# Kernel tuning notes

Measured on AMD Instinct MI355X. Metric: run time of the kernel, lower is better.

## Reference

```python
import jax, jax.numpy as jnp
import numpy as np

N = 50000      # nodes
E = 800000     # edges (avg degree 16)
F_IN = 64      # node_feature_dim
D = 128        # hidden_dim == output_dim
L = 3          # num_gnn_layers
B = 8          # number of graphs in the batch
GATE_H = 128   # GraphAttentionPool hidden_dim default


def _ln(x, g, b, eps=1e-5):
    m = x.mean(-1, keepdims=True)
    v = ((x - m) ** 2).mean(-1, keepdims=True)
    return (x - m) * jax.lax.rsqrt(v + eps) * g + b


def _gelu(x):
    return jax.nn.gelu(x, approximate=False)  # torch F.gelu default = exact erf


def setup_inputs() -> dict:
    key = jax.random.key(0)
    ks = jax.random.split(key, 12)
    p = lambda k, shape: (jax.random.normal(k, shape, jnp.float32) * 0.02)
    return {
        "x": jax.random.normal(ks[0], (N, F_IN), jnp.float32),
        "edge_index": jax.random.randint(ks[1], (2, E), 0, N, dtype=jnp.int32),
        "batch": jnp.sort(jax.random.randint(ks[2], (N,), 0, B, dtype=jnp.int32)),
        # input_proj: Linear + LayerNorm
        "w_in": p(ks[3], (F_IN, D)), "b_in": jnp.zeros((D,), jnp.float32),
        "ln_in_g": jnp.ones((D,), jnp.float32), "ln_in_b": jnp.zeros((D,), jnp.float32),
        # fallback GNN layers (stacked: all layers are 2D -> D)
        "gnn_w": p(ks[4], (L, 2 * D, D)), "gnn_b": jnp.zeros((L, D), jnp.float32),
        "gnn_ln_g": jnp.ones((L, D), jnp.float32), "gnn_ln_b": jnp.zeros((L, D), jnp.float32),
        # outer per-layer norms
        "norm_g": jnp.ones((L, D), jnp.float32), "norm_b": jnp.zeros((L, D), jnp.float32),
        # attention pool gate: Linear(D,128) -> tanh -> Linear(128,1)
        "gate_w1": p(ks[5], (D, GATE_H)), "gate_b1": jnp.zeros((GATE_H,), jnp.float32),
        "gate_w2": p(ks[6], (GATE_H,)), "gate_b2": jnp.zeros((), jnp.float32),
        # out_proj: Linear + LayerNorm + GELU
        "out_w": p(ks[7], (D, D)), "out_b": jnp.zeros((D,), jnp.float32),
        "out_ln_g": jnp.ones((D,), jnp.float32), "out_ln_b": jnp.zeros((D,), jnp.float32),
    }


def reference(x, edge_index, batch, w_in, b_in, ln_in_g, ln_in_b,
              gnn_w, gnn_b, gnn_ln_g, gnn_ln_b, norm_g, norm_b,
              gate_w1, gate_b1, gate_w2, gate_b2,
              out_w, out_b, out_ln_g, out_ln_b):
    src, dst = edge_index[0], edge_index[1]
    n = x.shape[0]

    # input_proj: Linear -> LayerNorm -> GELU
    h = _gelu(_ln(x @ w_in + b_in, ln_in_g, ln_in_b))

    # in-degree count (same every layer), clamped to >= 1
    deg = jax.ops.segment_sum(jnp.ones((src.shape[0],), h.dtype), dst, num_segments=n)
    deg = jnp.maximum(deg, 1.0)[:, None]  # (N, 1)

    for i in range(L):
        # mean-neighbor aggregation: gather x[src], scatter-add to dst
        agg = jax.ops.segment_sum(h[src], dst, num_segments=n) / deg  # (N, D)
        out = jnp.concatenate([h, agg], axis=-1) @ gnn_w[i] + gnn_b[i]
        h_new = _ln(_gelu(out), gnn_ln_g[i], gnn_ln_b[i])   # layer-internal norm
        h_new = _ln(h_new, norm_g[i], norm_b[i])             # outer norm
        if i < L - 1:
            h_new = _gelu(h_new) + h                         # residual (shapes match)
        h = h_new

    # attention pool (fallback path: global softmax over all nodes)
    gate_logits = jnp.tanh(h @ gate_w1 + gate_b1) @ gate_w2 + gate_b2  # (N,)
    gate = jax.nn.softmax(gate_logits, axis=0)
    pooled = jax.ops.segment_sum(h * gate[:, None], batch, num_segments=B)  # (B, D)

    spatial_embedding = _gelu(_ln(pooled @ out_w + out_b, out_ln_g, out_ln_b))
    return spatial_embedding, h, gate
```

## Files before the change

### kernel.cpp

```cpp
#include <hip/hip_runtime.h>
#include <math.h>

#define N_NODES 50000
#define N_EDGES 800000
#define F_IN 64
#define D 128
#define NLAYER 3
#define B_GRAPHS 8
#define GB 32
#define NPW 8
#define NBLK ((N_NODES + GB - 1) / GB)
#define SCAN_B 512
#define NPART ((N_NODES + SCAN_B - 1) / SCAN_B)
#define AGP 136

typedef float f32x4 __attribute__((ext_vector_type(4)));
typedef short bf16x8 __attribute__((ext_vector_type(8)));

__device__ __forceinline__ float gelu_exact(float x) {
    return 0.5f * x * (1.0f + erff(x * 0.7071067811865476f));
}

__device__ __forceinline__ unsigned short f2bf(float f) {
    unsigned int u = __float_as_uint(f);
    u = (u + 0x7fffu + ((u >> 16) & 1u)) >> 16;
    return (unsigned short)u;
}
__device__ __forceinline__ float bf2f(unsigned short u) {
    return __uint_as_float((unsigned int)u << 16);
}


__global__ void zero_int_kernel(int* __restrict__ p, int n) {
    int i = blockIdx.x * blockDim.x + threadIdx.x;
    int stride = gridDim.x * blockDim.x;
    for (; i < n; i += stride) p[i] = 0;
}

__global__ void degree_kernel(const int* __restrict__ dst, int* __restrict__ deg) {
    int e = blockIdx.x * blockDim.x + threadIdx.x;
    if (e < N_EDGES) atomicAdd(&deg[dst[e]], 1);
}

__global__ __launch_bounds__(SCAN_B) void scan_partials_kernel(const int* __restrict__ deg,
                                                               int* __restrict__ partials) {
    __shared__ int wsum[8];
    int tid = threadIdx.x;
    int lane = tid & 63, wave = tid >> 6;
    int i = blockIdx.x * SCAN_B + tid;
    int v = (i < N_NODES) ? deg[i] : 0;
    #pragma unroll
    for (int o = 32; o >= 1; o >>= 1) v += __shfl_xor(v, o);
    if (lane == 0) wsum[wave] = v;
    __syncthreads();
    if (tid == 0) {
        int t = 0;
        #pragma unroll
        for (int w = 0; w < 8; ++w) t += wsum[w];
        partials[blockIdx.x] = t;
    }
}

__global__ void scan_offsets_kernel(int* __restrict__ partials, int* __restrict__ row_ptr) {
    __shared__ int wtot[2];
    int tid = threadIdx.x;
    int lane = tid & 63, wave = tid >> 6;
    int v = (tid < NPART) ? partials[tid] : 0;
    int x = v;
    #pragma unroll
    for (int o = 1; o < 64; o <<= 1) { int nb = __shfl_up(x, o); if (lane >= o) x += nb; }
    if (lane == 63) wtot[wave] = x;
    __syncthreads();
    if (wave == 1) x += wtot[0];
    if (tid < NPART) partials[tid] = x - v;
    if (tid == 127) row_ptr[N_NODES] = x;
}

__global__ __launch_bounds__(SCAN_B) void scan_apply_kernel(const int* __restrict__ deg,
        const int* __restrict__ partials, int* __restrict__ row_ptr, int* __restrict__ cursor) {
    __shared__ int wsum[8];
    int tid = threadIdx.x;
    int lane = tid & 63, wave = tid >> 6;
    int i = blockIdx.x * SCAN_B + tid;
    int v = (i < N_NODES) ? deg[i] : 0;
    int x = v;
    #pragma unroll
    for (int o = 1; o < 64; o <<= 1) { int nb = __shfl_up(x, o); if (lane >= o) x += nb; }
    if (lane == 63) wsum[wave] = x;
    __syncthreads();
    int waveoff = 0;
    #pragma unroll
    for (int w = 0; w < 8; ++w) waveoff += (w < wave) ? wsum[w] : 0;
    int excl = partials[blockIdx.x] + waveoff + x - v;
    if (i < N_NODES) { row_ptr[i] = excl; cursor[i] = excl; }
}

__global__ void fill_kernel(const int* __restrict__ src, const int* __restrict__ dst,
                            int* __restrict__ cursor, int* __restrict__ csr) {
    int e = blockIdx.x * blockDim.x + threadIdx.x;
    if (e < N_EDGES) {
        int t = dst[e];
        int pos = atomicAdd(&cursor[t], 1);
        csr[pos] = src[e];
    }
}

#define WT_GNN (NLAYER * D * 2 * D)
#define WT_G1  (WT_GNN + D * D)
#define WT_ALL (WT_G1 + D * F_IN)
__global__ void wprep_kernel(const float* __restrict__ gnn_w, const float* __restrict__ gate_w1,
                             const float* __restrict__ w_in, unsigned short* __restrict__ wt,
                             float* __restrict__ pooled) {
    int idx = blockIdx.x * 256 + threadIdx.x;
    if (blockIdx.x == 0) {
        #pragma unroll
        for (int i = 0; i < 4; ++i) pooled[threadIdx.x + i * 256] = 0.f;
    }
    if (idx >= WT_ALL) return;
    if (idx < WT_GNN) {
        int l = idx / (D * 2 * D);
        int rem = idx - l * (D * 2 * D);
        int n = rem / (2 * D);
        int k = rem - n * (2 * D);
        wt[idx] = f2bf(gnn_w[(size_t)l * 2 * D * D + (size_t)k * D + n]);
    } else if (idx < WT_G1) {
        int rem = idx - WT_GNN;
        int n = rem / D;
        int k = rem - n * D;
        wt[idx] = f2bf(gate_w1[(size_t)k * D + n]);
    } else {
        int rem = idx - WT_G1;
        int n = rem / F_IN;
        int k = rem - n * F_IN;
        wt[idx] = f2bf(w_in[(size_t)k * D + n]);
    }
}


__global__ __launch_bounds__(256) void input_proj_v5(
        const float* __restrict__ x, const unsigned short* __restrict__ wti,
        const float* __restrict__ b, const float* __restrict__ gam,
        const float* __restrict__ bet, unsigned short* __restrict__ h16) {
    __shared__ float2 red[2][GB];
    int tid = threadIdx.x;
    int wave = tid >> 6, lane = tid & 63;
    int nblk0 = blockIdx.x * GB;
    int q = lane >> 4, c = lane & 15;
    int m0 = (wave >> 1) * 16;
    int n0 = (wave & 1) * 64;
    int mrow = nblk0 + m0 + c;
    int mclamp = (mrow < N_NODES) ? mrow : (N_NODES - 1);
    const float* xr = x + (size_t)mclamp * F_IN;

    f32x4 acc[4];
    #pragma unroll
    for (int t = 0; t < 4; ++t) {
        float bn = b[n0 + t * 16 + c];
        acc[t] = (f32x4){bn, bn, bn, bn};
    }
    #pragma unroll
    for (int kk = 0; kk < 2; ++kk) {
        float4 a0 = *(const float4*)&xr[kk * 32 + q * 8];
        float4 a1 = *(const float4*)&xr[kk * 32 + q * 8 + 4];
        bf16x8 av;
        av[0] = (short)f2bf(a0.x); av[1] = (short)f2bf(a0.y);
        av[2] = (short)f2bf(a0.z); av[3] = (short)f2bf(a0.w);
        av[4] = (short)f2bf(a1.x); av[5] = (short)f2bf(a1.y);
        av[6] = (short)f2bf(a1.z); av[7] = (short)f2bf(a1.w);
        #pragma unroll
        for (int t = 0; t < 4; ++t) {
            bf16x8 bv = *(const bf16x8*)&wti[(size_t)(n0 + t * 16 + c) * F_IN + kk * 32 + q * 8];
            acc[t] = __builtin_amdgcn_mfma_f32_16x16x32_bf16(av, bv, acc[t], 0, 0, 0);
        }
    }
    float s[4], sq[4];
    #pragma unroll
    for (int r = 0; r < 4; ++r) {
        s[r] = acc[0][r] + acc[1][r] + acc[2][r] + acc[3][r];
        sq[r] = acc[0][r] * acc[0][r] + acc[1][r] * acc[1][r]
              + acc[2][r] * acc[2][r] + acc[3][r] * acc[3][r];
    }
    #pragma unroll
    for (int o = 1; o <= 8; o <<= 1)
        #pragma unroll
        for (int r = 0; r < 4; ++r) { s[r] += __shfl_xor(s[r], o); sq[r] += __shfl_xor(sq[r], o); }
    if (c == 0) {
        #pragma unroll
        for (int r = 0; r < 4; ++r) red[wave & 1][m0 + q * 4 + r] = make_float2(s[r], sq[r]);
    }
    __syncthreads();
    float gv[4], bv2[4];
    #pragma unroll
    for (int t = 0; t < 4; ++t) {
        int nn = n0 + t * 16 + c;
        gv[t] = gam[nn]; bv2[t] = bet[nn];
    }
    #pragma unroll
    for (int r = 0; r < 4; ++r) {
        int m = m0 + q * 4 + r;
        int n = nblk0 + m;
        float2 p0 = red[0][m], p1 = red[1][m];
        float mean = (p0.x + p1.x) * (1.0f / D);
        float msq  = (p0.y + p1.y) * (1.0f / D);
        float istd = rsqrtf(msq - mean * mean + 1e-5f);
        if (n < N_NODES) {
            #pragma unroll
            for (int t = 0; t < 4; ++t) {
                int nn = n0 + t * 16 + c;
                float y = (acc[t][r] - mean) * istd * gv[t] + bv2[t];
                h16[(size_t)n * D + nn] = f2bf(gelu_exact(y));
            }
        }
    }
}


__device__ __forceinline__ void acc_row(float acc[8], bf16x8 v) {
    #pragma unroll
    for (int i = 0; i < 8; ++i)
        acc[i] += __uint_as_float(((unsigned int)(unsigned short)v[i]) << 16);
}

template<int DO_GATE>
__global__ __launch_bounds__(256) void gnn_layer_v7(
        const unsigned short* __restrict__ h16_in, unsigned short* __restrict__ h16_out,
        float* __restrict__ hf_out,
        const int* __restrict__ csr, const int* __restrict__ rp,
        const unsigned short* __restrict__ wt,
        const float* __restrict__ bias,
        const float* __restrict__ ln1g, const float* __restrict__ ln1b,
        const float* __restrict__ ln2g, const float* __restrict__ ln2b,
        int residual, int write_f32,
        const unsigned short* __restrict__ wtg,
        const float* __restrict__ gb1, const float* __restrict__ gw2,
        const float* __restrict__ gb2,
        float* __restrict__ logits, float2* __restrict__ gpart) {
    __shared__ int rps[GB + 1];
    __shared__ int eidx[GB][32];
    __shared__ unsigned short aggb[GB][AGP];
    __shared__ float2 red1[2][GB];
    __shared__ float2 red2[2][GB];
    __shared__ float redg[2][GB];
    __shared__ float lg[GB];

    int tid = threadIdx.x;
    int wave = tid >> 6, lane = tid & 63;
    int nblk0 = blockIdx.x * GB;
    int gbase = wave * NPW;

    if (tid < GB + 1) {
        int n = nblk0 + tid;
        if (n > N_NODES) n = N_NODES;
        rps[tid] = rp[n];
    }
    __syncthreads();
    #pragma unroll
    for (int k2 = 0; k2 < 4; ++k2) {
        int f = tid + k2 * 256;
        int g = f >> 5, sl = f & 31;
        int beg = rps[g], end = rps[g + 1];
        int ee = beg + sl;
        int ci = (ee < end) ? ee : ((end > beg) ? (end - 1) : 0);
        eidx[g][sl] = csr[ci];
    }
    __syncthreads();

    {
        int er = lane >> 4, dg = lane & 15;
        #pragma unroll
        for (int j = 0; j < NPW; ++j) {
            int g = gbase + j;
            int beg = rps[g], end = rps[g + 1];
            int deg = end - beg;
            int id8[8];
            #pragma unroll
            for (int t = 0; t < 8; ++t) id8[t] = eidx[g][er + 4 * t];
            bf16x8 v[8];
            #pragma unroll
            for (int t = 0; t < 8; ++t)
                v[t] = *(const bf16x8*)&h16_in[(size_t)id8[t] * D + dg * 8];
            float acc[8];
            #pragma unroll
            for (int i = 0; i < 8; ++i) acc[i] = 0.f;
            #pragma unroll
            for (int t = 0; t < 8; ++t)
                if (beg + er + 4 * t < end) acc_row(acc, v[t]);
            if (deg > 32) {
                for (int ee = beg + er + 32; ee < end; ee += 4) {
                    bf16x8 vv = *(const bf16x8*)&h16_in[(size_t)csr[ee] * D + dg * 8];
                    acc_row(acc, vv);
                }
            }
            #pragma unroll
            for (int i = 0; i < 8; ++i) {
                acc[i] += __shfl_xor(acc[i], 16);
                acc[i] += __shfl_xor(acc[i], 32);
            }
            float inv = 1.0f / fmaxf((float)deg, 1.0f);
            if (er == 0) {
                bf16x8 o;
                #pragma unroll
                for (int i = 0; i < 8; ++i) o[i] = (short)f2bf(acc[i] * inv);
                *(bf16x8*)&aggb[g][dg * 8] = o;
            }
        }
    }
    __syncthreads();

    int q = lane >> 4, c = lane & 15;
    int m0 = (wave >> 1) * 16;
    int n0 = (wave & 1) * 64;
    int mrow = nblk0 + m0 + c;
    int mclamp = (mrow < N_NODES) ? mrow : (N_NODES - 1);
    const unsigned short* arow = h16_in + (size_t)mclamp * D;

    f32x4 acc[4];
    #pragma unroll
    for (int t = 0; t < 4; ++t) {
        float bn = bias[n0 + t * 16 + c];
        acc[t] = (f32x4){bn, bn, bn, bn};
    }
    #pragma unroll
    for (int kk = 0; kk < 4; ++kk) {
        bf16x8 av = *(const bf16x8*)&arow[kk * 32 + q * 8];
        #pragma unroll
        for (int t = 0; t < 4; ++t) {
            bf16x8 bv = *(const bf16x8*)&wt[(size_t)(n0 + t * 16 + c) * 256 + kk * 32 + q * 8];
            acc[t] = __builtin_amdgcn_mfma_f32_16x16x32_bf16(av, bv, acc[t], 0, 0, 0);
        }
    }
    #pragma unroll
    for (int kk = 0; kk < 4; ++kk) {
        bf16x8 av = *(const bf16x8*)&aggb[m0 + c][kk * 32 + q * 8];
        #pragma unroll
        for (int t = 0; t < 4; ++t) {
            bf16x8 bv = *(const bf16x8*)&wt[(size_t)(n0 + t * 16 + c) * 256 + 128 + kk * 32 + q * 8];
            acc[t] = __builtin_amdgcn_mfma_f32_16x16x32_bf16(av, bv, acc[t], 0, 0, 0);
        }
    }

    float xv[4][4];
    #pragma unroll
    for (int t = 0; t < 4; ++t)
        #pragma unroll
        for (int r = 0; r < 4; ++r) xv[t][r] = gelu_exact(acc[t][r]);

    float s[4], sq[4];
    #pragma unroll
    for (int r = 0; r < 4; ++r) {
        s[r] = xv[0][r] + xv[1][r] + xv[2][r] + xv[3][r];
        sq[r] = xv[0][r] * xv[0][r] + xv[1][r] * xv[1][r] + xv[2][r] * xv[2][r] + xv[3][r] * xv[3][r];
    }
    #pragma unroll
    for (int o = 1; o <= 8; o <<= 1)
        #pragma unroll
        for (int r = 0; r < 4; ++r) { s[r] += __shfl_xor(s[r], o); sq[r] += __shfl_xor(sq[r], o); }
    int nh = wave & 1;
    if (c == 0) {
        #pragma unroll
        for (int r = 0; r < 4; ++r) red1[nh][m0 + q * 4 + r] = make_float2(s[r], sq[r]);
    }
    __syncthreads();

    float g1v[4], b1v[4], g2v[4], b2v[4];
    #pragma unroll
    for (int t = 0; t < 4; ++t) {
        int nn = n0 + t * 16 + c;
        g1v[t] = ln1g[nn]; b1v[t] = ln1b[nn];
        g2v[t] = ln2g[nn]; b2v[t] = ln2b[nn];
    }

    float y1[4][4];
    #pragma unroll
    for (int r = 0; r < 4; ++r) {
        int m = m0 + q * 4 + r;
        float2 p0 = red1[0][m], p1 = red1[1][m];
        float mean = (p0.x + p1.x) * (1.0f / D);
        float msq  = (p0.y + p1.y) * (1.0f / D);
        float istd = rsqrtf(msq - mean * mean + 1e-5f);
        #pragma unroll
        for (int t = 0; t < 4; ++t)
            y1[t][r] = (xv[t][r] - mean) * istd * g1v[t] + b1v[t];
    }

    #pragma unroll
    for (int r = 0; r < 4; ++r) {
        s[r] = y1[0][r] + y1[1][r] + y1[2][r] + y1[3][r];
        sq[r] = y1[0][r] * y1[0][r] + y1[1][r] * y1[1][r] + y1[2][r] * y1[2][r] + y1[3][r] * y1[3][r];
    }
    #pragma unroll
    for (int o = 1; o <= 8; o <<= 1)
        #pragma unroll
        for (int r = 0; r < 4; ++r) { s[r] += __shfl_xor(s[r], o); sq[r] += __shfl_xor(sq[r], o); }
    if (c == 0) {
        #pragma unroll
        for (int r = 0; r < 4; ++r) red2[nh][m0 + q * 4 + r] = make_float2(s[r], sq[r]);
    }
    __syncthreads();

    #pragma unroll
    for (int r = 0; r < 4; ++r) {
        int m = m0 + q * 4 + r;
        int n = nblk0 + m;
        float2 p0 = red2[0][m], p1 = red2[1][m];
        float mean = (p0.x + p1.x) * (1.0f / D);
        float msq  = (p0.y + p1.y) * (1.0f / D);
        float istd = rsqrtf(msq - mean * mean + 1e-5f);
        #pragma unroll
        for (int t = 0; t < 4; ++t) {
            int nn = n0 + t * 16 + c;
            float y2 = (y1[t][r] - mean) * istd * g2v[t] + b2v[t];
            float o = residual ? (gelu_exact(y2) + bf2f(h16_in[(size_t)n * D + nn])) : y2;
            if (n < N_NODES) {
                h16_out[(size_t)n * D + nn] = f2bf(o);
                if (write_f32) hf_out[(size_t)n * D + nn] = o;
            }
            if (DO_GATE) aggb[m][nn] = f2bf(o);
        }
    }

    if (DO_GATE) {
        __syncthreads();
        f32x4 gacc[4];
        #pragma unroll
        for (int t = 0; t < 4; ++t) {
            float bn = gb1[n0 + t * 16 + c];
            gacc[t] = (f32x4){bn, bn, bn, bn};
        }
        #pragma unroll
        for (int kk = 0; kk < 4; ++kk) {
            bf16x8 av = *(const bf16x8*)&aggb[m0 + c][kk * 32 + q * 8];
            #pragma unroll
            for (int t = 0; t < 4; ++t) {
                bf16x8 bv = *(const bf16x8*)&wtg[(size_t)(n0 + t * 16 + c) * 128 + kk * 32 + q * 8];
                gacc[t] = __builtin_amdgcn_mfma_f32_16x16x32_bf16(av, bv, gacc[t], 0, 0, 0);
            }
        }
        float w2v[4];
        #pragma unroll
        for (int t = 0; t < 4; ++t) w2v[t] = gw2[n0 + t * 16 + c];
        float gs[4];
        #pragma unroll
        for (int r = 0; r < 4; ++r) {
            gs[r] = tanhf(gacc[0][r]) * w2v[0] + tanhf(gacc[1][r]) * w2v[1]
                  + tanhf(gacc[2][r]) * w2v[2] + tanhf(gacc[3][r]) * w2v[3];
        }
        #pragma unroll
        for (int o = 1; o <= 8; o <<= 1)
            #pragma unroll
            for (int r = 0; r < 4; ++r) gs[r] += __shfl_xor(gs[r], o);
        if (c == 0) {
            #pragma unroll
            for (int r = 0; r < 4; ++r) redg[nh][m0 + q * 4 + r] = gs[r];
        }
        __syncthreads();
        if ((wave & 1) == 0 && c == 0) {
            float bb2 = gb2[0];
            #pragma unroll
            for (int r = 0; r < 4; ++r) {
                int m = m0 + q * 4 + r;
                int n = nblk0 + m;
                float L = redg[0][m] + redg[1][m] + bb2;
                if (n < N_NODES) { logits[n] = L; lg[m] = L; }
                else lg[m] = -INFINITY;
            }
        }
        __syncthreads();
        if (wave == 0) {
            float l = (lane < GB) ? lg[lane] : -INFINITY;
            float mx = l;
            #pragma unroll
            for (int o = 32; o >= 1; o >>= 1) mx = fmaxf(mx, __shfl_xor(mx, o));
            float ex = (lane < GB && l > -INFINITY) ? expf(l - mx) : 0.f;
            #pragma unroll
            for (int o = 32; o >= 1; o >>= 1) ex += __shfl_xor(ex, o);
            if (lane == 0) gpart[blockIdx.x] = make_float2(mx, ex);
        }
    }
}


#define POOL_CHUNK 128
__global__ __launch_bounds__(POOL_CHUNK) void gate_pool_v2(
        const unsigned short* __restrict__ h16, const float* __restrict__ logits,
        const float2* __restrict__ gpart, const int* __restrict__ batch,
        float* __restrict__ gate_out, float* __restrict__ pooled) {
    __shared__ float sb[4];
    __shared__ float gs[POOL_CHUNK];
    __shared__ int bs[POOL_CHUNK];
    int d = threadIdx.x;
    int lane = d & 63, wv = d >> 6;
    float mx = -INFINITY;
    for (int i = d; i < NBLK; i += POOL_CHUNK) mx = fmaxf(mx, gpart[i].x);
    #pragma unroll
    for (int o = 32; o >= 1; o >>= 1) mx = fmaxf(mx, __shfl_xor(mx, o));
    if (lane == 0) sb[wv] = mx;
    __syncthreads();
    mx = fmaxf(sb[0], sb[1]);
    float ssum = 0.f;
    for (int i = d; i < NBLK; i += POOL_CHUNK) {
        float2 p = gpart[i];
        ssum += p.y * expf(p.x - mx);
    }
    #pragma unroll
    for (int o = 32; o >= 1; o >>= 1) ssum += __shfl_xor(ssum, o);
    if (lane == 0) sb[2 + wv] = ssum;
    __syncthreads();
    float inv = 1.0f / (sb[2] + sb[3]);

    int n0 = blockIdx.x * POOL_CHUNK;
    int nj = n0 + d;
    if (nj < N_NODES) {
        float gv = expf(logits[nj] - mx) * inv;
        gs[d] = gv;
        bs[d] = batch[nj];
        gate_out[nj] = gv;
    }
    __syncthreads();
    int count = min(POOL_CHUNK, N_NODES - n0);
    float acc = 0.f;
    int cur = bs[0];
    int t = 0;
    for (; t + 3 < count; t += 4) {
        float h0 = bf2f(h16[(size_t)(n0 + t + 0) * D + d]);
        float h1 = bf2f(h16[(size_t)(n0 + t + 1) * D + d]);
        float h2 = bf2f(h16[(size_t)(n0 + t + 2) * D + d]);
        float h3 = bf2f(h16[(size_t)(n0 + t + 3) * D + d]);
        int b0 = bs[t], b1 = bs[t + 1], b2 = bs[t + 2], b3 = bs[t + 3];
        if (b0 != cur) { atomicAdd(&pooled[cur * D + d], acc); acc = 0.f; cur = b0; }
        acc = fmaf(h0, gs[t], acc);
        if (b1 != cur) { atomicAdd(&pooled[cur * D + d], acc); acc = 0.f; cur = b1; }
        acc = fmaf(h1, gs[t + 1], acc);
        if (b2 != cur) { atomicAdd(&pooled[cur * D + d], acc); acc = 0.f; cur = b2; }
        acc = fmaf(h2, gs[t + 2], acc);
        if (b3 != cur) { atomicAdd(&pooled[cur * D + d], acc); acc = 0.f; cur = b3; }
        acc = fmaf(h3, gs[t + 3], acc);
    }
    for (; t < count; ++t) {
        int bn = bs[t];
        if (bn != cur) { atomicAdd(&pooled[cur * D + d], acc); acc = 0.f; cur = bn; }
        acc = fmaf(bf2f(h16[(size_t)(n0 + t) * D + d]), gs[t], acc);
    }
    atomicAdd(&pooled[cur * D + d], acc);
}

__global__ void out_proj_kernel(const float* __restrict__ pooled, const float* __restrict__ w,
                                const float* __restrict__ b, const float* __restrict__ g,
                                const float* __restrict__ beta, float* __restrict__ emb) {
    __shared__ float ps[D];
    __shared__ float sbuf[2];
    int bg = blockIdx.x, d = threadIdx.x;
    ps[d] = pooled[bg * D + d];
    __syncthreads();
    float acc = b[d];
    #pragma unroll 8
    for (int k = 0; k < D; ++k) acc += ps[k] * w[k * D + d];
    float s = acc, q = acc * acc;
    #pragma unroll
    for (int o = 32; o >= 1; o >>= 1) { s += __shfl_down(s, o); q += __shfl_down(q, o); }
    if ((d & 63) == 0) { sbuf[d >> 6] = s; }
    __syncthreads();
    float fullsum = sbuf[0] + sbuf[1];
    __syncthreads();
    if ((d & 63) == 0) { sbuf[d >> 6] = q; }
    __syncthreads();
    float fullsq = sbuf[0] + sbuf[1];
    float m = fullsum * (1.0f / D);
    float var = fullsq * (1.0f / D) - m * m;
    float y = (acc - m) * rsqrtf(var + 1e-5f) * g[d] + beta[d];
    emb[bg * D + d] = gelu_exact(y);
}

extern "C" void kernel_launch(void* const* d_in, const int* in_sizes, int n_in,
                              void* d_out, int out_size, void* d_ws, size_t ws_size,
                              hipStream_t stream) {
    const float* x        = (const float*)d_in[0];
    const int*   edge     = (const int*)d_in[1];
    const int*   batch    = (const int*)d_in[2];
    const float* w_in     = (const float*)d_in[3];
    const float* b_in     = (const float*)d_in[4];
    const float* ln_in_g  = (const float*)d_in[5];
    const float* ln_in_b  = (const float*)d_in[6];
    const float* gnn_w    = (const float*)d_in[7];
    const float* gnn_b    = (const float*)d_in[8];
    const float* gnn_ln_g = (const float*)d_in[9];
    const float* gnn_ln_b = (const float*)d_in[10];
    const float* norm_g   = (const float*)d_in[11];
    const float* norm_b   = (const float*)d_in[12];
    const float* gate_w1  = (const float*)d_in[13];
    const float* gate_b1  = (const float*)d_in[14];
    const float* gate_w2  = (const float*)d_in[15];
    const float* gate_b2  = (const float*)d_in[16];
    const float* out_w    = (const float*)d_in[17];
    const float* out_b    = (const float*)d_in[18];
    const float* out_ln_g = (const float*)d_in[19];
    const float* out_ln_b = (const float*)d_in[20];

    const int* src = edge;
    const int* dst = edge + N_EDGES;

    float* out      = (float*)d_out;
    float* emb      = out;
    float* hA       = out + B_GRAPHS * D;
    float* gate_out = hA + (size_t)N_NODES * D;

    unsigned short* h16A = (unsigned short*)d_ws;
    unsigned short* h16B = h16A + (size_t)N_NODES * D;
    int*   deg_i    = (int*)d_ws;
    int*   cursor   = (int*)d_ws + N_NODES;
    int*   row_ptr  = (int*)(h16B + (size_t)N_NODES * D);
    int*   csr      = row_ptr + N_NODES + 1;
    float* logits   = (float*)(csr + N_EDGES);
    float* pooled   = logits + N_NODES;
    int*   partials = (int*)(pooled + B_GRAPHS * D);
    float2* gpart   = (float2*)(((uintptr_t)(partials + NPART) + 15) & ~(uintptr_t)15);
    unsigned short* wt  = (unsigned short*)(gpart + NBLK);
    unsigned short* wtg = wt + WT_GNN;
    unsigned short* wti = wt + WT_G1;

    zero_int_kernel<<<128, 256, 0, stream>>>(deg_i, N_NODES);
    degree_kernel<<<(N_EDGES + 255) / 256, 256, 0, stream>>>(dst, deg_i);
    scan_partials_kernel<<<NPART, SCAN_B, 0, stream>>>(deg_i, partials);
    scan_offsets_kernel<<<1, 128, 0, stream>>>(partials, row_ptr);
    scan_apply_kernel<<<NPART, SCAN_B, 0, stream>>>(deg_i, partials, row_ptr, cursor);
    fill_kernel<<<(N_EDGES + 255) / 256, 256, 0, stream>>>(src, dst, cursor, csr);
    wprep_kernel<<<(WT_ALL + 255) / 256, 256, 0, stream>>>(gnn_w, gate_w1, w_in, wt, pooled);

    input_proj_v5<<<NBLK, 256, 0, stream>>>(x, wti, b_in, ln_in_g, ln_in_b, h16B);

    gnn_layer_v7<0><<<NBLK, 256, 0, stream>>>(
        h16B, h16A, hA, csr, row_ptr, wt, gnn_b,
        gnn_ln_g, gnn_ln_b, norm_g, norm_b, 1, 0,
        nullptr, nullptr, nullptr, nullptr, nullptr, nullptr);
    gnn_layer_v7<0><<<NBLK, 256, 0, stream>>>(
        h16A, h16B, hA, csr, row_ptr, wt + (size_t)1 * D * 2 * D, gnn_b + D,
        gnn_ln_g + D, gnn_ln_b + D, norm_g + D, norm_b + D, 1, 0,
        nullptr, nullptr, nullptr, nullptr, nullptr, nullptr);
    gnn_layer_v7<1><<<NBLK, 256, 0, stream>>>(
        h16B, h16A, hA, csr, row_ptr, wt + (size_t)2 * D * 2 * D, gnn_b + 2 * D,
        gnn_ln_g + 2 * D, gnn_ln_b + 2 * D, norm_g + 2 * D, norm_b + 2 * D, 0, 1,
        wtg, gate_b1, gate_w2, gate_b2, logits, gpart);

    gate_pool_v2<<<(N_NODES + POOL_CHUNK - 1) / POOL_CHUNK, POOL_CHUNK, 0, stream>>>(
        h16A, logits, gpart, batch, gate_out, pooled);
    out_proj_kernel<<<B_GRAPHS, D, 0, stream>>>(pooled, out_w, out_b, out_ln_g, out_ln_b, emb);
}
```

Baseline: 454.0 us.

## Double-buffer neighbor gathers via direct global-to-LDS async loads

The neighbor aggregation in the GNN layer kernel now issues global_load_lds transfers into a per-wave double-buffered LDS staging area, prefetching the next node's 32 neighbor rows while the current one is reduced. Manual vmcnt waits pace the pipeline, and per-node row offsets are hoisted into scalar registers with readfirstlane. This aims to hide gather latency and free registers. In exchange it adds 64KB of shared memory per block, which may reduce occupancy, and the hand-written waitcnt logic is fragile if the compiler adds other outstanding vector loads.

```diff
diff --git a/kernel.cpp b/kernel.cpp
--- a/kernel.cpp
+++ b/kernel.cpp
@@ -16,6 +16,9 @@
 
 typedef float f32x4 __attribute__((ext_vector_type(4)));
 typedef short bf16x8 __attribute__((ext_vector_type(8)));
+
+typedef const __attribute__((address_space(1))) unsigned int* gas_u32p;
+typedef __attribute__((address_space(3))) unsigned int* las_u32p;
 
 __device__ __forceinline__ float gelu_exact(float x) {
     return 0.5f * x * (1.0f + erff(x * 0.7071067811865476f));
@@ -221,8 +224,10 @@
         acc[i] += __uint_as_float(((unsigned int)(unsigned short)v[i]) << 16);
 }
 
+#define STG_ROWS 32
+
 template<int DO_GATE>
-__global__ __launch_bounds__(256) void gnn_layer_v7(
+__global__ __launch_bounds__(256) void gnn_layer_v9(
         const unsigned short* __restrict__ h16_in, unsigned short* __restrict__ h16_out,
         float* __restrict__ hf_out,
         const int* __restrict__ csr, const int* __restrict__ rp,
@@ -235,6 +240,7 @@
         const float* __restrict__ gb1, const float* __restrict__ gw2,
         const float* __restrict__ gb2,
         float* __restrict__ logits, float2* __restrict__ gpart) {
+    __shared__ unsigned short stg[4][2][STG_ROWS][D];
     __shared__ int rps[GB + 1];
     __shared__ int eidx[GB][32];
     __shared__ unsigned short aggb[GB][AGP];
@@ -267,41 +273,65 @@
 
     {
         int er = lane >> 4, dg = lane & 15;
+
+        int bj[NPW + 1];
+        #pragma unroll
+        for (int j = 0; j <= NPW; ++j)
+            bj[j] = __builtin_amdgcn_readfirstlane(rps[gbase + j]);
+        int dj[NPW];
+        #pragma unroll
+        for (int j = 0; j < NPW; ++j) dj[j] = bj[j + 1] - bj[j];
+
+        auto issue_node = [&](int g, int buf) {
+            #pragma unroll
+            for (int t = 0; t < 8; ++t) {
+                int id_ = eidx[g][4 * t + er];
+                const unsigned short* gp = h16_in + (size_t)id_ * D + dg * 8;
+                __builtin_amdgcn_global_load_lds(
+                    (gas_u32p)(const void*)gp,
+                    (las_u32p)(void*)&stg[wave][buf][4 * t][0],
+                    16, 0, 0);
+            }
+        };
+
+        issue_node(gbase + 0, 0);
+        issue_node(gbase + 1, 1);
+
         #pragma unroll
         for (int j = 0; j < NPW; ++j) {
-            int g = gbase + j;
-            int beg = rps[g], end = rps[g + 1];
-            int deg = end - beg;
-            int id8[8];
-            #pragma unroll
-            for (int t = 0; t < 8; ++t) id8[t] = eidx[g][er + 4 * t];
-            bf16x8 v[8];
-            #pragma unroll
-            for (int t = 0; t < 8; ++t)
-                v[t] = *(const bf16x8*)&h16_in[(size_t)id8[t] * D + dg * 8];
+            const int buf = j & 1;
+            if (j < NPW - 1) asm volatile("s_waitcnt vmcnt(8)" ::: "memory");
+            else             asm volatile("s_waitcnt vmcnt(0)" ::: "memory");
+
+            int deg_s = dj[j];
             float acc[8];
             #pragma unroll
             for (int i = 0; i < 8; ++i) acc[i] = 0.f;
             #pragma unroll
-            for (int t = 0; t < 8; ++t)
-                if (beg + er + 4 * t < end) acc_row(acc, v[t]);
-            if (deg > 32) {
-                for (int ee = beg + er + 32; ee < end; ee += 4) {
+            for (int t = 0; t < 8; ++t) {
+                bf16x8 v = *(const bf16x8*)&stg[wave][buf][4 * t + er][dg * 8];
+                if (er + 4 * t < deg_s) acc_row(acc, v);
+            }
+            if (deg_s > 32) {
+                int beg_s = bj[j], end_s = bj[j] + deg_s;
+                for (int ee = beg_s + er + 32; ee < end_s; ee += 4) {
                     bf16x8 vv = *(const bf16x8*)&h16_in[(size_t)csr[ee] * D + dg * 8];
                     acc_row(acc, vv);
                 }
             }
+            if (j + 2 < NPW) issue_node(gbase + j + 2, buf);
+
             #pragma unroll
             for (int i = 0; i < 8; ++i) {
                 acc[i] += __shfl_xor(acc[i], 16);
                 acc[i] += __shfl_xor(acc[i], 32);
             }
-            float inv = 1.0f / fmaxf((float)deg, 1.0f);
+            float inv = 1.0f / fmaxf((float)deg_s, 1.0f);
             if (er == 0) {
                 bf16x8 o;
                 #pragma unroll
                 for (int i = 0; i < 8; ++i) o[i] = (short)f2bf(acc[i] * inv);
-                *(bf16x8*)&aggb[g][dg * 8] = o;
+                *(bf16x8*)&aggb[gbase + j][dg * 8] = o;
             }
         }
     }
@@ -628,15 +658,15 @@
 
     input_proj_v5<<<NBLK, 256, 0, stream>>>(x, wti, b_in, ln_in_g, ln_in_b, h16B);
 
-    gnn_layer_v7<0><<<NBLK, 256, 0, stream>>>(
+    gnn_layer_v9<0><<<NBLK, 256, 0, stream>>>(
         h16B, h16A, hA, csr, row_ptr, wt, gnn_b,
         gnn_ln_g, gnn_ln_b, norm_g, norm_b, 1, 0,
         nullptr, nullptr, nullptr, nullptr, nullptr, nullptr);
-    gnn_layer_v7<0><<<NBLK, 256, 0, stream>>>(
+    gnn_layer_v9<0><<<NBLK, 256, 0, stream>>>(
         h16A, h16B, hA, csr, row_ptr, wt + (size_t)1 * D * 2 * D, gnn_b + D,
         gnn_ln_g + D, gnn_ln_b + D, norm_g + D, norm_b + D, 1, 0,
         nullptr, nullptr, nullptr, nullptr, nullptr, nullptr);
-    gnn_layer_v7<1><<<NBLK, 256, 0, stream>>>(
+    gnn_layer_v9<1><<<NBLK, 256, 0, stream>>>(
         h16B, h16A, hA, csr, row_ptr, wt + (size_t)2 * D * 2 * D, gnn_b + 2 * D,
         gnn_ln_g + 2 * D, gnn_ln_b + 2 * D, norm_g + 2 * D, norm_b + 2 * D, 0, 1,
         wtg, gate_b1, gate_w2, gate_b2, logits, gpart);
```

Measured after the change: 535.8 us. +18.0%, slower.

## Double GNN layer block to 512 threads, splitting gather and MFMA columns across 8 waves

Applied to the files above, without the earlier changes.

The fused GNN layer kernel now runs 512 threads (8 waves) per 32-node block instead of 256. Each wave gathers neighbors for 4 nodes instead of 8 and computes a 16x32 output tile instead of 16x64. The LayerNorm and gate reductions are widened to combine four partial sums. The aim is more memory-level parallelism in the latency-bound neighbor gather and fewer registers per wave, at the cost of more block-level synchronization and reduction traffic.

```diff
diff --git a/kernel.cpp b/kernel.cpp
--- a/kernel.cpp
+++ b/kernel.cpp
@@ -8,7 +8,8 @@
 #define NLAYER 3
 #define B_GRAPHS 8
 #define GB 32
-#define NPW 8
+#define BTH 512
+#define NPW2 4
 #define NBLK ((N_NODES + GB - 1) / GB)
 #define SCAN_B 512
 #define NPART ((N_NODES + SCAN_B - 1) / SCAN_B)
@@ -222,7 +223,7 @@
 }
 
 template<int DO_GATE>
-__global__ __launch_bounds__(256) void gnn_layer_v7(
+__global__ __launch_bounds__(BTH, 8) void gnn_layer_v10(
         const unsigned short* __restrict__ h16_in, unsigned short* __restrict__ h16_out,
         float* __restrict__ hf_out,
         const int* __restrict__ csr, const int* __restrict__ rp,
@@ -238,15 +239,14 @@
     __shared__ int rps[GB + 1];
     __shared__ int eidx[GB][32];
     __shared__ unsigned short aggb[GB][AGP];
-    __shared__ float2 red1[2][GB];
-    __shared__ float2 red2[2][GB];
-    __shared__ float redg[2][GB];
+    __shared__ float2 red1[4][GB];
+    __shared__ float2 red2[4][GB];
+    __shared__ float redg[4][GB];
     __shared__ float lg[GB];
 
     int tid = threadIdx.x;
     int wave = tid >> 6, lane = tid & 63;
     int nblk0 = blockIdx.x * GB;
-    int gbase = wave * NPW;
 
     if (tid < GB + 1) {
         int n = nblk0 + tid;
@@ -255,8 +255,8 @@
     }
     __syncthreads();
     #pragma unroll
-    for (int k2 = 0; k2 < 4; ++k2) {
-        int f = tid + k2 * 256;
+    for (int k2 = 0; k2 < 2; ++k2) {
+        int f = tid + k2 * BTH;
         int g = f >> 5, sl = f & 31;
         int beg = rps[g], end = rps[g + 1];
         int ee = beg + sl;
@@ -267,8 +267,9 @@
 
     {
         int er = lane >> 4, dg = lane & 15;
-        #pragma unroll
-        for (int j = 0; j < NPW; ++j) {
+        int gbase = wave * NPW2;
+        #pragma unroll
+        for (int j = 0; j < NPW2; ++j) {
             int g = gbase + j;
             int beg = rps[g], end = rps[g + 1];
             int deg = end - beg;
@@ -308,15 +309,15 @@
     __syncthreads();
 
     int q = lane >> 4, c = lane & 15;
-    int m0 = (wave >> 1) * 16;
-    int n0 = (wave & 1) * 64;
+    int m0 = (wave >> 2) * 16;
+    int n0 = (wave & 3) * 32;
     int mrow = nblk0 + m0 + c;
     int mclamp = (mrow < N_NODES) ? mrow : (N_NODES - 1);
     const unsigned short* arow = h16_in + (size_t)mclamp * D;
 
-    f32x4 acc[4];
-    #pragma unroll
-    for (int t = 0; t < 4; ++t) {
+    f32x4 acc[2];
+    #pragma unroll
+    for (int t = 0; t < 2; ++t) {
         float bn = bias[n0 + t * 16 + c];
         acc[t] = (f32x4){bn, bn, bn, bn};
     }
@@ -324,7 +325,7 @@
     for (int kk = 0; kk < 4; ++kk) {
         bf16x8 av = *(const bf16x8*)&arow[kk * 32 + q * 8];
         #pragma unroll
-        for (int t = 0; t < 4; ++t) {
+        for (int t = 0; t < 2; ++t) {
             bf16x8 bv = *(const bf16x8*)&wt[(size_t)(n0 + t * 16 + c) * 256 + kk * 32 + q * 8];
             acc[t] = __builtin_amdgcn_mfma_f32_16x16x32_bf16(av, bv, acc[t], 0, 0, 0);
         }
@@ -333,60 +334,60 @@
     for (int kk = 0; kk < 4; ++kk) {
         bf16x8 av = *(const bf16x8*)&aggb[m0 + c][kk * 32 + q * 8];
         #pragma unroll
-        for (int t = 0; t < 4; ++t) {
+        for (int t = 0; t < 2; ++t) {
             bf16x8 bv = *(const bf16x8*)&wt[(size_t)(n0 + t * 16 + c) * 256 + 128 + kk * 32 + q * 8];
             acc[t] = __builtin_amdgcn_mfma_f32_16x16x32_bf16(av, bv, acc[t], 0, 0, 0);
         }
     }
 
-    float xv[4][4];
-    #pragma unroll
-    for (int t = 0; t < 4; ++t)
+    float xv[2][4];
+    #pragma unroll
+    for (int t = 0; t < 2; ++t)
         #pragma unroll
         for (int r = 0; r < 4; ++r) xv[t][r] = gelu_exact(acc[t][r]);
 
     float s[4], sq[4];
     #pragma unroll
     for (int r = 0; r < 4; ++r) {
-        s[r] = xv[0][r] + xv[1][r] + xv[2][r] + xv[3][r];
-        sq[r] = xv[0][r] * xv[0][r] + xv[1][r] * xv[1][r] + xv[2][r] * xv[2][r] + xv[3][r] * xv[3][r];
+        s[r] = xv[0][r] + xv[1][r];
+        sq[r] = xv[0][r] * xv[0][r] + xv[1][r] * xv[1][r];
     }
     #pragma unroll
     for (int o = 1; o <= 8; o <<= 1)
         #pragma unroll
         for (int r = 0; r < 4; ++r) { s[r] += __shfl_xor(s[r], o); sq[r] += __shfl_xor(sq[r], o); }
-    int nh = wave & 1;
+    int nh = wave & 3;
     if (c == 0) {
         #pragma unroll
         for (int r = 0; r < 4; ++r) red1[nh][m0 + q * 4 + r] = make_float2(s[r], sq[r]);
     }
     __syncthreads();
 
-    float g1v[4], b1v[4], g2v[4], b2v[4];
-    #pragma unroll
-    for (int t = 0; t < 4; ++t) {
+    float g1v[2], b1v[2], g2v[2], b2v[2];
+    #pragma unroll
+    for (int t = 0; t < 2; ++t) {
         int nn = n0 + t * 16 + c;
         g1v[t] = ln1g[nn]; b1v[t] = ln1b[nn];
         g2v[t] = ln2g[nn]; b2v[t] = ln2b[nn];
     }
 
-    float y1[4][4];
+    float y1[2][4];
     #pragma unroll
     for (int r = 0; r < 4; ++r) {
         int m = m0 + q * 4 + r;
-        float2 p0 = red1[0][m], p1 = red1[1][m];
-        float mean = (p0.x + p1.x) * (1.0f / D);
-        float msq  = (p0.y + p1.y) * (1.0f / D);
+        float2 p0 = red1[0][m], p1 = red1[1][m], p2 = red1[2][m], p3 = red1[3][m];
+        float mean = (p0.x + p1.x + p2.x + p3.x) * (1.0f / D);
+        float msq  = (p0.y + p1.y + p2.y + p3.y) * (1.0f / D);
         float istd = rsqrtf(msq - mean * mean + 1e-5f);
         #pragma unroll
-        for (int t = 0; t < 4; ++t)
+        for (int t = 0; t < 2; ++t)
             y1[t][r] = (xv[t][r] - mean) * istd * g1v[t] + b1v[t];
     }
 
     #pragma unroll
     for (int r = 0; r < 4; ++r) {
-        s[r] = y1[0][r] + y1[1][r] + y1[2][r] + y1[3][r];
-        sq[r] = y1[0][r] * y1[0][r] + y1[1][r] * y1[1][r] + y1[2][r] * y1[2][r] + y1[3][r] * y1[3][r];
+        s[r] = y1[0][r] + y1[1][r];
+        sq[r] = y1[0][r] * y1[0][r] + y1[1][r] * y1[1][r];
     }
     #pragma unroll
     for (int o = 1; o <= 8; o <<= 1)
@@ -402,12 +403,12 @@
     for (int r = 0; r < 4; ++r) {
         int m = m0 + q * 4 + r;
         int n = nblk0 + m;
-        float2 p0 = red2[0][m], p1 = red2[1][m];
-        float mean = (p0.x + p1.x) * (1.0f / D);
-        float msq  = (p0.y + p1.y) * (1.0f / D);
+        float2 p0 = red2[0][m], p1 = red2[1][m], p2 = red2[2][m], p3 = red2[3][m];
+        float mean = (p0.x + p1.x + p2.x + p3.x) * (1.0f / D);
+        float msq  = (p0.y + p1.y + p2.y + p3.y) * (1.0f / D);
         float istd = rsqrtf(msq - mean * mean + 1e-5f);
         #pragma unroll
-        for (int t = 0; t < 4; ++t) {
+        for (int t = 0; t < 2; ++t) {
             int nn = n0 + t * 16 + c;
             float y2 = (y1[t][r] - mean) * istd * g2v[t] + b2v[t];
             float o = residual ? (gelu_exact(y2) + bf2f(h16_in[(size_t)n * D + nn])) : y2;
@@ -421,9 +422,9 @@
 
     if (DO_GATE) {
         __syncthreads();
-        f32x4 gacc[4];
-        #pragma unroll
-        for (int t = 0; t < 4; ++t) {
+        f32x4 gacc[2];
+        #pragma unroll
+        for (int t = 0; t < 2; ++t) {
             float bn = gb1[n0 + t * 16 + c];
             gacc[t] = (f32x4){bn, bn, bn, bn};
         }
@@ -431,20 +432,18 @@
         for (int kk = 0; kk < 4; ++kk) {
             bf16x8 av = *(const bf16x8*)&aggb[m0 + c][kk * 32 + q * 8];
             #pragma unroll
-            for (int t = 0; t < 4; ++t) {
+            for (int t = 0; t < 2; ++t) {
                 bf16x8 bv = *(const bf16x8*)&wtg[(size_t)(n0 + t * 16 + c) * 128 + kk * 32 + q * 8];
                 gacc[t] = __builtin_amdgcn_mfma_f32_16x16x32_bf16(av, bv, gacc[t], 0, 0, 0);
             }
         }
-        float w2v[4];
-        #pragma unroll
-        for (int t = 0; t < 4; ++t) w2v[t] = gw2[n0 + t * 16 + c];
+        float w2v[2];
+        #pragma unroll
+        for (int t = 0; t < 2; ++t) w2v[t] = gw2[n0 + t * 16 + c];
         float gs[4];
         #pragma unroll
-        for (int r = 0; r < 4; ++r) {
-            gs[r] = tanhf(gacc[0][r]) * w2v[0] + tanhf(gacc[1][r]) * w2v[1]
-                  + tanhf(gacc[2][r]) * w2v[2] + tanhf(gacc[3][r]) * w2v[3];
-        }
+        for (int r = 0; r < 4; ++r)
+            gs[r] = tanhf(gacc[0][r]) * w2v[0] + tanhf(gacc[1][r]) * w2v[1];
         #pragma unroll
         for (int o = 1; o <= 8; o <<= 1)
             #pragma unroll
@@ -454,13 +453,13 @@
             for (int r = 0; r < 4; ++r) redg[nh][m0 + q * 4 + r] = gs[r];
         }
         __syncthreads();
-        if ((wave & 1) == 0 && c == 0) {
+        if ((wave & 3) == 0 && c == 0) {
             float bb2 = gb2[0];
             #pragma unroll
             for (int r = 0; r < 4; ++r) {
                 int m = m0 + q * 4 + r;
                 int n = nblk0 + m;
-                float L = redg[0][m] + redg[1][m] + bb2;
+                float L = redg[0][m] + redg[1][m] + redg[2][m] + redg[3][m] + bb2;
                 if (n < N_NODES) { logits[n] = L; lg[m] = L; }
                 else lg[m] = -INFINITY;
             }
@@ -628,15 +627,15 @@
 
     input_proj_v5<<<NBLK, 256, 0, stream>>>(x, wti, b_in, ln_in_g, ln_in_b, h16B);
 
-    gnn_layer_v7<0><<<NBLK, 256, 0, stream>>>(
+    gnn_layer_v10<0><<<NBLK, BTH, 0, stream>>>(
         h16B, h16A, hA, csr, row_ptr, wt, gnn_b,
         gnn_ln_g, gnn_ln_b, norm_g, norm_b, 1, 0,
         nullptr, nullptr, nullptr, nullptr, nullptr, nullptr);
-    gnn_layer_v7<0><<<NBLK, 256, 0, stream>>>(
+    gnn_layer_v10<0><<<NBLK, BTH, 0, stream>>>(
         h16A, h16B, hA, csr, row_ptr, wt + (size_t)1 * D * 2 * D, gnn_b + D,
         gnn_ln_g + D, gnn_ln_b + D, norm_g + D, norm_b + D, 1, 0,
         nullptr, nullptr, nullptr, nullptr, nullptr, nullptr);
-    gnn_layer_v7<1><<<NBLK, 256, 0, stream>>>(
+    gnn_layer_v10<1><<<NBLK, BTH, 0, stream>>>(
         h16B, h16A, hA, csr, row_ptr, wt + (size_t)2 * D * 2 * D, gnn_b + 2 * D,
         gnn_ln_g + 2 * D, gnn_ln_b + 2 * D, norm_g + 2 * D, norm_b + 2 * D, 0, 1,
         wtg, gate_b1, gate_w2, gate_b2, logits, gpart);
```

Result: no change. 460.7 us (+1.5%).
